# Optimization experiments

Measured on AMD Instinct MI355X. Metric: run time of the kernel, lower is better.

The kernel has to match this reference:

```python
import math
import jax, jax.numpy as jnp
import numpy as np

DIM = 256
DENOM = 10000.0
MAX_LENGTH = 1000
SEQ_IN = 1024
BATCH = 32
MAX_DUR = 8


def make_encoding():
    # encoding[p, 0::2] = sin(p * div), encoding[p, 1::2] = cos(p * div)
    pos = jnp.arange(MAX_LENGTH, dtype=jnp.float32)[:, None]              # (L, 1)
    div = jnp.exp(jnp.arange(0, DIM, 2, dtype=jnp.float32) * (-math.log(DENOM) / DIM))  # (D/2,)
    sin = jnp.sin(pos * div)                                              # (L, D/2)
    cos = jnp.cos(pos * div)                                              # (L, D/2)
    return jnp.stack([sin, cos], axis=-1).reshape(MAX_LENGTH, DIM)        # interleaved


def setup_inputs() -> dict:
    key = jax.random.key(0)
    durations = jax.random.randint(key, (SEQ_IN, BATCH), 0, MAX_DUR, dtype=jnp.int32)
    encoding = make_encoding()
    return {"durations": durations, "encoding": encoding}


def reference(durations, encoding):
    # durations: (S, B) int; encoding: (L, D)
    S, B = durations.shape
    cum = jnp.cumsum(durations, axis=0)          # (S, B) exclusive-end offsets
    starts = cum - durations                     # (S, B) start offset of each token
    total = cum[-1]                              # (B,) total frames per batch element
    T_out = int(jnp.max(total))                  # pad_sequence pads to longest sequence

    frames = jnp.arange(T_out, dtype=cum.dtype)  # (T,)
    # token owning frame i: first t with cum[t] > i (skips zero-duration tokens)
    token = jax.vmap(lambda c: jnp.searchsorted(c, frames, side='right'))(cum.T)  # (B, T)
    token_c = jnp.clip(token, 0, S - 1)
    pos = frames[None, :] - jnp.take_along_axis(starts.T, token_c, axis=1)        # (B, T)
    valid = frames[None, :] < total[:, None]                                      # (B, T)

    pos = jnp.clip(pos, 0, encoding.shape[0] - 1)
    emb = encoding[pos]                                                           # (B, T, D)
    emb = jnp.where(valid[..., None], emb, jnp.zeros((), emb.dtype))
    return jnp.transpose(emb, (1, 0, 2))                                          # (T, B, D)
```

## Files before the change

kernel.cpp:

```cpp
#include <hip/hip_runtime.h>

#define SEQ   1024
#define BATCH 32
#define DIM   256

__global__ __launch_bounds__(256) void pe_scan_scatter(const int* __restrict__ dur,
                                                       int* __restrict__ pos,
                                                       int* __restrict__ totals,
                                                       int T) {
    const int b = blockIdx.x;
    const int t = threadIdx.x;
    __shared__ int ssum[256];

    int d[4];
    const int base = (t * 4) * BATCH + b;
#pragma unroll
    for (int i = 0; i < 4; ++i) d[i] = dur[base + i * BATCH];

    ssum[t] = d[0] + d[1] + d[2] + d[3];
    __syncthreads();

    for (int off = 1; off < 256; off <<= 1) {
        int v = (t >= off) ? ssum[t - off] : 0;
        __syncthreads();
        ssum[t] += v;
        __syncthreads();
    }

    if (t == 255) totals[b] = ssum[255];

    int start = (t > 0) ? ssum[t - 1] : 0;
#pragma unroll
    for (int i = 0; i < 4; ++i) {
        for (int k = 0; k < d[i]; ++k) {
            int f = start + k;
            if (f < T) pos[f * BATCH + b] = k;
        }
        start += d[i];
    }
}

__global__ __launch_bounds__(256) void pe_gather(const int* __restrict__ pos,
                                                 const int* __restrict__ totals,
                                                 const float4* __restrict__ enc,
                                                 float4* __restrict__ out,
                                                 int n4) {
    int idx = blockIdx.x * blockDim.x + threadIdx.x;
    if (idx >= n4) return;
    int row = idx >> 6;
    int f   = row >> 5;
    int b   = row & 31;
    float4 v = {0.f, 0.f, 0.f, 0.f};
    if (f < totals[b]) {
        int p = pos[row];
        v = enc[p * (DIM / 4) + (idx & 63)];
    }
    out[idx] = v;
}

extern "C" void kernel_launch(void* const* d_in, const int* in_sizes, int n_in,
                              void* d_out, int out_size, void* d_ws, size_t ws_size,
                              hipStream_t stream) {
    const int*   dur = (const int*)d_in[0];
    const float* enc = (const float*)d_in[1];
    float*       out = (float*)d_out;

    const int T     = out_size / (BATCH * DIM);
    const int nrows = T * BATCH;
    int* pos    = (int*)d_ws;
    int* totals = pos + nrows;

    pe_scan_scatter<<<BATCH, 256, 0, stream>>>(dur, pos, totals, T);

    const int n4 = nrows * (DIM / 4);
    pe_gather<<<(n4 + 255) / 256, 256, 0, stream>>>(
        pos, totals, (const float4*)enc, (float4*)out, n4);
}
```

Measured before the change: 132.7 us.

## Use byte positions, 1024-thread scan, and nontemporal output stores

The scan kernel now uses one thread per token with a 1024-entry shared scan, which removes the per-thread serial loop over four tokens. Positions are stored as bytes in batch-major order, which shrinks the intermediate buffer. The gather kernel writes its output with nontemporal stores to reduce cache pollution on the large write stream. Storing positions as bytes relies on durations being under 256, and each output row now reads its position with a strided access.

```diff
diff --git a/kernel.cpp b/kernel.cpp
--- a/kernel.cpp
+++ b/kernel.cpp
@@ -4,58 +4,53 @@
 #define BATCH 32
 #define DIM   256
 
-__global__ __launch_bounds__(256) void pe_scan_scatter(const int* __restrict__ dur,
-                                                       int* __restrict__ pos,
-                                                       int* __restrict__ totals,
-                                                       int T) {
+typedef float vfloat4 __attribute__((ext_vector_type(4)));
+
+__global__ __launch_bounds__(1024) void pe_scan_scatter(const int* __restrict__ dur,
+                                                        unsigned char* __restrict__ pos8,
+                                                        int* __restrict__ totals,
+                                                        int T) {
     const int b = blockIdx.x;
     const int t = threadIdx.x;
-    __shared__ int ssum[256];
+    __shared__ int ssum[SEQ];
 
-    int d[4];
-    const int base = (t * 4) * BATCH + b;
-#pragma unroll
-    for (int i = 0; i < 4; ++i) d[i] = dur[base + i * BATCH];
-
-    ssum[t] = d[0] + d[1] + d[2] + d[3];
+    const int d = dur[t * BATCH + b];
+    ssum[t] = d;
     __syncthreads();
 
-    for (int off = 1; off < 256; off <<= 1) {
+    for (int off = 1; off < SEQ; off <<= 1) {
         int v = (t >= off) ? ssum[t - off] : 0;
         __syncthreads();
         ssum[t] += v;
         __syncthreads();
     }
 
-    if (t == 255) totals[b] = ssum[255];
+    if (t == SEQ - 1) totals[b] = ssum[t];
 
-    int start = (t > 0) ? ssum[t - 1] : 0;
-#pragma unroll
-    for (int i = 0; i < 4; ++i) {
-        for (int k = 0; k < d[i]; ++k) {
-            int f = start + k;
-            if (f < T) pos[f * BATCH + b] = k;
-        }
-        start += d[i];
+    int start = ssum[t] - d;
+    unsigned char* dst = pos8 + (size_t)b * T;
+    for (int k = 0; k < d; ++k) {
+        int f = start + k;
+        if (f < T) dst[f] = (unsigned char)k;
     }
 }
 
-__global__ __launch_bounds__(256) void pe_gather(const int* __restrict__ pos,
+__global__ __launch_bounds__(256) void pe_gather(const unsigned char* __restrict__ pos8,
                                                  const int* __restrict__ totals,
-                                                 const float4* __restrict__ enc,
-                                                 float4* __restrict__ out,
-                                                 int n4) {
+                                                 const vfloat4* __restrict__ enc,
+                                                 vfloat4* __restrict__ out,
+                                                 int n4, int T) {
     int idx = blockIdx.x * blockDim.x + threadIdx.x;
     if (idx >= n4) return;
     int row = idx >> 6;
     int f   = row >> 5;
     int b   = row & 31;
-    float4 v = {0.f, 0.f, 0.f, 0.f};
+    vfloat4 v = {0.f, 0.f, 0.f, 0.f};
     if (f < totals[b]) {
-        int p = pos[row];
+        int p = pos8[(size_t)b * T + f];
         v = enc[p * (DIM / 4) + (idx & 63)];
     }
-    out[idx] = v;
+    __builtin_nontemporal_store(v, &out[idx]);
 }
 
 extern "C" void kernel_launch(void* const* d_in, const int* in_sizes, int n_in,
@@ -63,16 +58,15 @@
                               hipStream_t stream) {
     const int*   dur = (const int*)d_in[0];
     const float* enc = (const float*)d_in[1];
-    float*       out = (float*)d_out;
 
-    const int T     = out_size / (BATCH * DIM);
-    const int nrows = T * BATCH;
-    int* pos    = (int*)d_ws;
-    int* totals = pos + nrows;
+    const int T = out_size / (BATCH * DIM);
 
-    pe_scan_scatter<<<BATCH, 256, 0, stream>>>(dur, pos, totals, T);
+    int*           totals = (int*)d_ws;
+    unsigned char* pos8   = (unsigned char*)d_ws + 128;
 
-    const int n4 = nrows * (DIM / 4);
+    pe_scan_scatter<<<BATCH, 1024, 0, stream>>>(dur, pos8, totals, T);
+
+    const int n4 = T * BATCH * (DIM / 4);
     pe_gather<<<(n4 + 255) / 256, 256, 0, stream>>>(
-        pos, totals, (const float4*)enc, (float4*)out, n4);
+        pos8, totals, (const vfloat4*)enc, (vfloat4*)d_out, n4, T);
 }
```

After: 132.9 us. About the same (+0.1%).
